# Kernel optimization log

Hardware: AMD Instinct MI355X
Metric: run time of the kernel (lower is better)

## Reference

```python
import jax, jax.numpy as jnp
import numpy as np

B, F, V, E = 65536, 39, 100000, 16
EPS = 1e-5

def setup_inputs() -> dict:
    key = jax.random.key(0)
    ks = jax.random.split(key, 10)
    return {
        'Xi': jax.random.randint(ks[0], (B, F, 1), 0, V, dtype=jnp.int64) if jax.config.read('jax_enable_x64') else jax.random.randint(ks[0], (B, F, 1), 0, V, dtype=jnp.int32),
        'Xv': jax.random.uniform(ks[1], (B, F), dtype=jnp.float32),
        'emb1': jax.random.normal(ks[2], (F, V, 1), dtype=jnp.float32),
        'emb2': jax.random.normal(ks[3], (F, V, E), dtype=jnp.float32),
        'W1': jax.random.normal(ks[4], (F * E, 512), dtype=jnp.float32) * 0.02,
        'b1': jax.random.normal(ks[5], (512,), dtype=jnp.float32) * 0.02,
        'g1': jnp.ones((512,), jnp.float32),
        'be1': jnp.zeros((512,), jnp.float32),
        'W2': jax.random.normal(ks[6], (512, 256), dtype=jnp.float32) * 0.02,
        'b2': jax.random.normal(ks[7], (256,), dtype=jnp.float32) * 0.02,
        'g2': jnp.ones((256,), jnp.float32),
        'be2': jnp.zeros((256,), jnp.float32),
        'bias': jax.random.normal(ks[8], (1,), dtype=jnp.float32),
    }

def _batchnorm(x, g, b):
    mu = jnp.mean(x, axis=0)
    var = jnp.mean(jnp.square(x - mu), axis=0)  # biased var, torch BN training mode
    return (x - mu) * jax.lax.rsqrt(var + EPS) * g + b

def reference(Xi, Xv, emb1, emb2, W1, b1, g1, be1, W2, b2, g2, be2, bias):
    idx = Xi[:, :, 0]                                # [B, F]
    fidx = jnp.arange(F)[None, :]                    # [1, F]
    # fused per-field gathers: [B, F] and [B, F, E]
    first = emb1[fidx, idx, 0] * Xv                  # first-order, [B, F]
    fm2 = emb2[fidx, idx] * Xv[:, :, None]           # second-order embeds, [B, F, E]
    sum_emb = jnp.sum(fm2, axis=1)                   # [B, E]
    second = 0.5 * (jnp.square(sum_emb) - jnp.sum(jnp.square(fm2), axis=1))  # [B, E]
    # deep part (note: original forward never applies the final num_classes layer)
    deep = fm2.reshape(B, F * E)
    deep = _batchnorm(deep @ W1 + b1, g1, be1)
    deep = _batchnorm(deep @ W2 + b2, g2, be2)
    return bias + jnp.sum(first, axis=1) + jnp.sum(second, axis=1) + jnp.sum(deep, axis=1)
```

## Files before the change

### kernel.cpp

```cpp
#include <hip/hip_runtime.h>

#define B_ROWS 65536
#define F_FEAT 39
#define V_VOC  100000
#define D_PAD  640
#define BN_EPS 1e-5f

typedef __bf16 bf16x8 __attribute__((ext_vector_type(8)));
typedef float  f32x16 __attribute__((ext_vector_type(16)));

__device__ __forceinline__ unsigned short toBF(float x) {
  unsigned int u = __float_as_uint(x);
  u += 0x7fffu + ((u >> 16) & 1u);
  return (unsigned short)(u >> 16);
}

__global__ __launch_bounds__(256) void k1_gather(
    const int* __restrict__ Xi, const float* __restrict__ Xv,
    const float* __restrict__ emb2,
    unsigned short* __restrict__ XT, float* __restrict__ fs,
    float* __restrict__ Mz) {
  if (threadIdx.x < 100)
    Mz[(size_t)blockIdx.x * 100 + threadIdx.x] = 0.f;

  const int b0 = blockIdx.x * 16;
  __shared__ int            sIdx[16][40];
  __shared__ float          sXv[16][40];
  __shared__ unsigned short xt[16][648];

  for (int u = threadIdx.x; u < 16 * 39; u += 256) {
    int r = u / 39, f = u - r * 39;
    sIdx[r][f] = Xi[(size_t)(b0 + r) * 39 + f];
    sXv[r][f]  = Xv[(size_t)(b0 + r) * 39 + f];
  }
  __syncthreads();

  const int r   = threadIdx.x >> 4;
  const int l16 = threadIdx.x & 15;
  const int seg = l16 & 3;
  const int fo  = l16 >> 2;

  float4 sv = {0.f, 0.f, 0.f, 0.f};
  float  ss = 0.f;
#pragma unroll
  for (int it = 0; it < 10; ++it) {
    const int f = it * 4 + fo;
    if (f < 39) {
      const int   id = sIdx[r][f];
      const float xv = sXv[r][f];
      const float4 v = *reinterpret_cast<const float4*>(
          emb2 + ((size_t)f * V_VOC + id) * 16 + seg * 4);
      const float a0 = v.x * xv, a1 = v.y * xv, a2 = v.z * xv, a3 = v.w * xv;
      sv.x += a0; sv.y += a1; sv.z += a2; sv.w += a3;
      ss += a0 * a0 + a1 * a1 + a2 * a2 + a3 * a3;
      uint2 pk;
      pk.x = (unsigned int)toBF(a0) | ((unsigned int)toBF(a1) << 16);
      pk.y = (unsigned int)toBF(a2) | ((unsigned int)toBF(a3) << 16);
      *reinterpret_cast<uint2*>(&xt[r][f * 16 + seg * 4]) = pk;
    }
  }
  sv.x += __shfl_xor(sv.x, 4); sv.y += __shfl_xor(sv.y, 4);
  sv.z += __shfl_xor(sv.z, 4); sv.w += __shfl_xor(sv.w, 4);
  sv.x += __shfl_xor(sv.x, 8); sv.y += __shfl_xor(sv.y, 8);
  sv.z += __shfl_xor(sv.z, 8); sv.w += __shfl_xor(sv.w, 8);
  float s2 = sv.x * sv.x + sv.y * sv.y + sv.z * sv.z + sv.w * sv.w;
  s2 += __shfl_xor(s2, 1);
  s2 += __shfl_xor(s2, 2);
  ss += __shfl_xor(ss, 1);
  ss += __shfl_xor(ss, 2);
  ss += __shfl_xor(ss, 4);
  ss += __shfl_xor(ss, 8);
  if (l16 == 0) fs[b0 + r] = 0.5f * (s2 - ss);
  __syncthreads();

  for (int m = threadIdx.x; m < 640; m += 256) {
    unsigned short* dst = XT + (size_t)m * B_ROWS + b0;
    unsigned int q2[8];
    if (m < 624) {
#pragma unroll
      for (int rr = 0; rr < 8; ++rr)
        q2[rr] = (unsigned int)xt[2 * rr][m] | ((unsigned int)xt[2 * rr + 1][m] << 16);
    } else {
      unsigned int fill = (m == 624) ? 0x3f803f80u : 0u;
#pragma unroll
      for (int rr = 0; rr < 8; ++rr) q2[rr] = fill;
    }
    uint4 w0, w1;
    w0.x = q2[0]; w0.y = q2[1]; w0.z = q2[2]; w0.w = q2[3];
    w1.x = q2[4]; w1.y = q2[5]; w1.z = q2[6]; w1.w = q2[7];
    *reinterpret_cast<uint4*>(dst)     = w0;
    *reinterpret_cast<uint4*>(dst + 8) = w1;
  }
}

#define KSPLIT 32
__global__ __launch_bounds__(256) void k2_syrk(const unsigned short* __restrict__ XT,
                                               float* __restrict__ M) {
  const int ks = blockIdx.x & (KSPLIT - 1);
  int pair = blockIdx.x >> 5;
  int ti = 0, p = pair;
  while (p >= 5 - ti) { p -= 5 - ti; ++ti; }
  const int tj = ti + p;

  __shared__ unsigned short pa[128 * 64];
  __shared__ unsigned short pb[128 * 64];

  const int lane = threadIdx.x & 63, wid = threadIdx.x >> 6;
  const int wm = wid >> 1, wn = wid & 1;
  const int rl = lane & 31, hh = lane >> 5;

  f32x16 acc00, acc01, acc10, acc11;
#pragma unroll
  for (int i = 0; i < 16; ++i) { acc00[i] = 0.f; acc01[i] = 0.f; acc10[i] = 0.f; acc11[i] = 0.f; }

  const int krange = B_ROWS / KSPLIT;
  const int kbase = ks * krange;

  for (int kt = 0; kt < krange; kt += 64) {
    const int k0 = kbase + kt;
#pragma unroll
    for (int g2 = 0; g2 < 4; ++g2) {
      const int g = threadIdx.x + g2 * 256;
      const int r = g >> 3, j = g & 7;
      uint4 va = *reinterpret_cast<const uint4*>(XT + (size_t)(ti * 128 + r) * B_ROWS + k0 + j * 8);
      *reinterpret_cast<uint4*>((char*)pa + r * 128 + ((j ^ (r & 7)) << 4)) = va;
      uint4 vb = *reinterpret_cast<const uint4*>(XT + (size_t)(tj * 128 + r) * B_ROWS + k0 + j * 8);
      *reinterpret_cast<uint4*>((char*)pb + r * 128 + ((j ^ (r & 7)) << 4)) = vb;
    }
    __syncthreads();
#pragma unroll
    for (int kc = 0; kc < 4; ++kc) {
      const int ra0 = wm * 64 + rl, ra1 = wm * 64 + 32 + rl;
      const int rb0 = wn * 64 + rl, rb1 = wn * 64 + 32 + rl;
      bf16x8 a0 = *reinterpret_cast<const bf16x8*>((char*)pa + ra0 * 128 + (((kc * 2 + hh) ^ (ra0 & 7)) << 4));
      bf16x8 a1 = *reinterpret_cast<const bf16x8*>((char*)pa + ra1 * 128 + (((kc * 2 + hh) ^ (ra1 & 7)) << 4));
      bf16x8 b0 = *reinterpret_cast<const bf16x8*>((char*)pb + rb0 * 128 + (((kc * 2 + hh) ^ (rb0 & 7)) << 4));
      bf16x8 b1 = *reinterpret_cast<const bf16x8*>((char*)pb + rb1 * 128 + (((kc * 2 + hh) ^ (rb1 & 7)) << 4));
      acc00 = __builtin_amdgcn_mfma_f32_32x32x16_bf16(a0, b0, acc00, 0, 0, 0);
      acc01 = __builtin_amdgcn_mfma_f32_32x32x16_bf16(a0, b1, acc01, 0, 0, 0);
      acc10 = __builtin_amdgcn_mfma_f32_32x32x16_bf16(a1, b0, acc10, 0, 0, 0);
      acc11 = __builtin_amdgcn_mfma_f32_32x32x16_bf16(a1, b1, acc11, 0, 0, 0);
    }
    __syncthreads();
  }

#pragma unroll
  for (int rr = 0; rr < 16; ++rr) {
    const int rloc = (rr & 3) + ((rr >> 2) << 3) + hh * 4;
    const int row0 = ti * 128 + wm * 64 + rloc;
    const int row1 = row0 + 32;
    const int col0 = tj * 128 + wn * 64 + rl;
    atomicAdd(&M[row0 * D_PAD + col0], acc00[rr]);
    atomicAdd(&M[row0 * D_PAD + col0 + 32], acc01[rr]);
    atomicAdd(&M[row1 * D_PAD + col0], acc10[rr]);
    atomicAdd(&M[row1 * D_PAD + col0 + 32], acc11[rr]);
  }
}

__device__ __forceinline__ float fetchM(const float* M, int a, int b) {
  if ((a >> 7) > (b >> 7)) { int t = a; a = b; b = t; }
  return M[a * D_PAD + b];
}
__global__ void k3a_cov(const float* __restrict__ M, float* __restrict__ Cov,
                        float* __restrict__ mu) {
  const int i = blockIdx.x;
  const float inv = 1.f / 65536.f;
  const float mui = fetchM(M, 624, i) * inv;
  for (int j = threadIdx.x; j < D_PAD; j += 256) {
    float muj = fetchM(M, 624, j) * inv;
    Cov[i * D_PAD + j] = fetchM(M, i, j) * inv - mui * muj;
    if (i == 0) mu[j] = muj;
  }
}

__global__ __launch_bounds__(256) void qform(const float* __restrict__ Cov,
                                             const float* __restrict__ W, const int ldw,
                                             const float* __restrict__ g,
                                             float* __restrict__ alpha) {
  const int k0 = blockIdx.x * 2;
  __shared__ float w0s[624], w1s[624];
  for (int i = threadIdx.x; i < 624; i += 256) {
    w0s[i] = W[(size_t)i * ldw + k0];
    w1s[i] = W[(size_t)i * ldw + k0 + 1];
  }
  __syncthreads();
  const int j0 = threadIdx.x, j1 = threadIdx.x + 256, j2 = threadIdx.x + 512;
  const bool v2 = (j2 < 624);
  const float wj00 = w0s[j0], wj01 = w0s[j1], wj02 = v2 ? w0s[j2] : 0.f;
  const float wj10 = w1s[j0], wj11 = w1s[j1], wj12 = v2 ? w1s[j2] : 0.f;
  float acc0 = 0.f, acc1 = 0.f;
  for (int i = 0; i < 624; ++i) {
    const float wi0 = w0s[i], wi1 = w1s[i];
    const float* row = Cov + i * D_PAD;
    const float c0 = row[j0], c1 = row[j1], c2 = v2 ? row[j2] : 0.f;
    acc0 += wi0 * (c0 * wj00 + c1 * wj01 + c2 * wj02);
    acc1 += wi1 * (c0 * wj10 + c1 * wj11 + c2 * wj12);
  }
#pragma unroll
  for (int off = 32; off > 0; off >>= 1) {
    acc0 += __shfl_down(acc0, off);
    acc1 += __shfl_down(acc1, off);
  }
  __shared__ float pr[2][4];
  const int lane = threadIdx.x & 63, wv = threadIdx.x >> 6;
  if (lane == 0) { pr[0][wv] = acc0; pr[1][wv] = acc1; }
  __syncthreads();
  if (threadIdx.x == 0) {
    float v0 = pr[0][0] + pr[0][1] + pr[0][2] + pr[0][3];
    float v1 = pr[1][0] + pr[1][1] + pr[1][2] + pr[1][3];
    alpha[k0]     = g[k0]     * rsqrtf(v0 + BN_EPS);
    alpha[k0 + 1] = g[k0 + 1] * rsqrtf(v1 + BN_EPS);
  }
}

__global__ __launch_bounds__(256) void k3c_G(const float* __restrict__ W1,
                                             const float* __restrict__ alpha1,
                                             const float* __restrict__ W2,
                                             float* __restrict__ G) {
  const int i = blockIdx.x;
  __shared__ float a[512];
  for (int k = threadIdx.x; k < 512; k += 256)
    a[k] = W1[(size_t)i * 512 + k] * alpha1[k];
  __syncthreads();
  const int j = threadIdx.x;
  float acc = 0.f;
#pragma unroll 8
  for (int k = 0; k < 512; ++k) acc += a[k] * W2[(size_t)k * 256 + j];
  G[(size_t)i * 256 + j] = acc;
}

__global__ __launch_bounds__(256) void k3e_final(const float* __restrict__ G,
                                                 const float* __restrict__ alpha2,
                                                 const float* __restrict__ mu,
                                                 const float* __restrict__ be2,
                                                 const float* __restrict__ bias,
                                                 float* __restrict__ gw,
                                                 float* __restrict__ consts) {
  __shared__ float a2[256];
  __shared__ float gws[640];
  a2[threadIdx.x] = alpha2[threadIdx.x];
  __syncthreads();
  for (int i = threadIdx.x; i < 640; i += 256) {
    float acc = 0.f;
    if (i < 624) {
      const float* gr = G + (size_t)i * 256;
#pragma unroll 8
      for (int j = 0; j < 256; ++j) acc += gr[j] * a2[j];
    }
    gw[i] = acc;
    gws[i] = acc;
  }
  __syncthreads();
  float pm = 0.f;
  for (int i = threadIdx.x; i < 624; i += 256) pm += mu[i] * gws[i];
  float val = be2[threadIdx.x] - pm;
#pragma unroll
  for (int off = 32; off > 0; off >>= 1) val += __shfl_down(val, off);
  __shared__ float pr[4];
  const int lane = threadIdx.x & 63, wv = threadIdx.x >> 6;
  if (lane == 0) pr[wv] = val;
  __syncthreads();
  if (threadIdx.x == 0) consts[0] = bias[0] + pr[0] + pr[1] + pr[2] + pr[3];
}

__global__ __launch_bounds__(256) void k5_out(const int* __restrict__ Xi,
                                              const float* __restrict__ Xv,
                                              const float* __restrict__ emb1,
                                              const unsigned short* __restrict__ XT,
                                              const float* __restrict__ gw,
                                              const float* __restrict__ fs,
                                              const float* __restrict__ consts,
                                              float* __restrict__ out) {
  const int b0 = blockIdx.x * 128;
  __shared__ int   si[128][40];
  __shared__ float sx[128][40];
  __shared__ float g[624];
  for (int m = threadIdx.x; m < 624; m += 256) g[m] = gw[m];
  for (int u = threadIdx.x; u < 128 * 39; u += 256) {
    int rr = u / 39, ff = u - rr * 39;
    si[rr][ff] = Xi[(size_t)b0 * 39 + u];
    sx[rr][ff] = Xv[(size_t)b0 * 39 + u];
  }
  __syncthreads();
  const int r = threadIdx.x >> 1, h = threadIdx.x & 1;
  const int b = b0 + r;
  float acc = 0.f;
  const unsigned short* col = XT + b;
  const int m0 = h * 312;
#pragma unroll 8
  for (int m = m0; m < m0 + 312; ++m) {
    unsigned int u = (unsigned int)col[(size_t)m * B_ROWS] << 16;
    acc += __uint_as_float(u) * g[m];
  }
  const int fb = h ? 20 : 0, fe = h ? 39 : 20;
  for (int f = fb; f < fe; ++f)
    acc += emb1[(size_t)f * V_VOC + si[r][f]] * sx[r][f];
  acc += __shfl_xor(acc, 1);
  if (h == 0) out[b] = acc + fs[b] + consts[0];
}

extern "C" void kernel_launch(void* const* d_in, const int* in_sizes, int n_in,
                              void* d_out, int out_size, void* d_ws, size_t ws_size,
                              hipStream_t stream) {
  const int*   Xi   = (const int*)d_in[0];
  const float* Xv   = (const float*)d_in[1];
  const float* emb1 = (const float*)d_in[2];
  const float* emb2 = (const float*)d_in[3];
  const float* W1   = (const float*)d_in[4];
  const float* g1   = (const float*)d_in[6];
  const float* W2   = (const float*)d_in[8];
  const float* g2   = (const float*)d_in[10];
  const float* be2  = (const float*)d_in[11];
  const float* bias = (const float*)d_in[12];
  float* out = (float*)d_out;
  char* ws = (char*)d_ws;

  const size_t OFF_XT  = 0;
  const size_t OFF_M   = OFF_XT + (size_t)640 * 65536 * 2;
  const size_t OFF_COV = OFF_M + (size_t)640 * 640 * 4;
  const size_t OFF_MU  = OFF_COV + (size_t)640 * 640 * 4;
  const size_t OFF_A1  = OFF_MU + 640 * 4;
  const size_t OFF_A2  = OFF_A1 + 512 * 4;
  const size_t OFF_G   = OFF_A2 + 256 * 4;
  const size_t OFF_GW  = OFF_G + (size_t)624 * 256 * 4;
  const size_t OFF_CN  = OFF_GW + 640 * 4;
  const size_t OFF_FS  = OFF_CN + 256;

  unsigned short* XT = (unsigned short*)(ws + OFF_XT);
  float* M   = (float*)(ws + OFF_M);
  float* COV = (float*)(ws + OFF_COV);
  float* MU  = (float*)(ws + OFF_MU);
  float* A1  = (float*)(ws + OFF_A1);
  float* A2  = (float*)(ws + OFF_A2);
  float* G   = (float*)(ws + OFF_G);
  float* GW  = (float*)(ws + OFF_GW);
  float* CN  = (float*)(ws + OFF_CN);
  float* FS  = (float*)(ws + OFF_FS);

  k1_gather<<<4096, 256, 0, stream>>>(Xi, Xv, emb2, XT, FS, M);
  k2_syrk<<<15 * KSPLIT, 256, 0, stream>>>(XT, M);
  k3a_cov<<<640, 256, 0, stream>>>(M, COV, MU);
  qform<<<256, 256, 0, stream>>>(COV, W1, 512, g1, A1);
  k3c_G<<<624, 256, 0, stream>>>(W1, A1, W2, G);
  qform<<<128, 256, 0, stream>>>(COV, G, 256, g2, A2);
  k3e_final<<<1, 256, 0, stream>>>(G, A2, MU, be2, bias, GW, CN);
  k5_out<<<512, 256, 0, stream>>>(Xi, Xv, emb1, XT, GW, FS, CN, out);
}
```

Before: 360.4 us.

## Restructure embedding gather per field, move FM second-order term into output kernel

Adds a prep kernel that transposes Xi/Xv into field-major layout, zeroes M and fills the padding rows of XT. The gather becomes one block per field and batch chunk, so each block reads from a single field's embedding table with software prefetch and writes coalesced transposed bf16 rows through a double-buffered shared tile. The FM second-order sum moves into k5_out, computed from the bf16 XT values, which drops the fs buffer but lowers the precision of that term. The syrk block index mapping is also changed to spread the K-splits across XCDs.

```diff
diff --git a/kernel.cpp b/kernel.cpp
--- a/kernel.cpp
+++ b/kernel.cpp
@@ -15,92 +15,89 @@
   return (unsigned short)(u >> 16);
 }
 
-__global__ __launch_bounds__(256) void k1_gather(
+__global__ __launch_bounds__(256) void k0_prep(
     const int* __restrict__ Xi, const float* __restrict__ Xv,
-    const float* __restrict__ emb2,
-    unsigned short* __restrict__ XT, float* __restrict__ fs,
-    float* __restrict__ Mz) {
-  if (threadIdx.x < 100)
-    Mz[(size_t)blockIdx.x * 100 + threadIdx.x] = 0.f;
-
-  const int b0 = blockIdx.x * 16;
-  __shared__ int            sIdx[16][40];
-  __shared__ float          sXv[16][40];
-  __shared__ unsigned short xt[16][648];
-
-  for (int u = threadIdx.x; u < 16 * 39; u += 256) {
+    int* __restrict__ XiT, float* __restrict__ XvT,
+    float* __restrict__ M, unsigned short* __restrict__ XT) {
+  for (int i = threadIdx.x; i < 800; i += 256)
+    M[(size_t)blockIdx.x * 800 + i] = 0.f;
+
+  const int b0 = blockIdx.x * 128;
+  for (int u = threadIdx.x; u < 16 * 128; u += 256) {
+    int m = 624 + (u >> 7), j = u & 127;
+    XT[(size_t)m * B_ROWS + b0 + j] = (m == 624) ? (unsigned short)0x3f80 : (unsigned short)0;
+  }
+
+  __shared__ int   ti[128][41];
+  __shared__ float tv[128][41];
+  for (int u = threadIdx.x; u < 128 * 39; u += 256) {
     int r = u / 39, f = u - r * 39;
-    sIdx[r][f] = Xi[(size_t)(b0 + r) * 39 + f];
-    sXv[r][f]  = Xv[(size_t)(b0 + r) * 39 + f];
-  }
-  __syncthreads();
-
-  const int r   = threadIdx.x >> 4;
-  const int l16 = threadIdx.x & 15;
-  const int seg = l16 & 3;
-  const int fo  = l16 >> 2;
-
-  float4 sv = {0.f, 0.f, 0.f, 0.f};
-  float  ss = 0.f;
-#pragma unroll
-  for (int it = 0; it < 10; ++it) {
-    const int f = it * 4 + fo;
-    if (f < 39) {
-      const int   id = sIdx[r][f];
-      const float xv = sXv[r][f];
-      const float4 v = *reinterpret_cast<const float4*>(
-          emb2 + ((size_t)f * V_VOC + id) * 16 + seg * 4);
-      const float a0 = v.x * xv, a1 = v.y * xv, a2 = v.z * xv, a3 = v.w * xv;
-      sv.x += a0; sv.y += a1; sv.z += a2; sv.w += a3;
-      ss += a0 * a0 + a1 * a1 + a2 * a2 + a3 * a3;
-      uint2 pk;
-      pk.x = (unsigned int)toBF(a0) | ((unsigned int)toBF(a1) << 16);
-      pk.y = (unsigned int)toBF(a2) | ((unsigned int)toBF(a3) << 16);
-      *reinterpret_cast<uint2*>(&xt[r][f * 16 + seg * 4]) = pk;
-    }
-  }
-  sv.x += __shfl_xor(sv.x, 4); sv.y += __shfl_xor(sv.y, 4);
-  sv.z += __shfl_xor(sv.z, 4); sv.w += __shfl_xor(sv.w, 4);
-  sv.x += __shfl_xor(sv.x, 8); sv.y += __shfl_xor(sv.y, 8);
-  sv.z += __shfl_xor(sv.z, 8); sv.w += __shfl_xor(sv.w, 8);
-  float s2 = sv.x * sv.x + sv.y * sv.y + sv.z * sv.z + sv.w * sv.w;
-  s2 += __shfl_xor(s2, 1);
-  s2 += __shfl_xor(s2, 2);
-  ss += __shfl_xor(ss, 1);
-  ss += __shfl_xor(ss, 2);
-  ss += __shfl_xor(ss, 4);
-  ss += __shfl_xor(ss, 8);
-  if (l16 == 0) fs[b0 + r] = 0.5f * (s2 - ss);
-  __syncthreads();
-
-  for (int m = threadIdx.x; m < 640; m += 256) {
-    unsigned short* dst = XT + (size_t)m * B_ROWS + b0;
-    unsigned int q2[8];
-    if (m < 624) {
-#pragma unroll
-      for (int rr = 0; rr < 8; ++rr)
-        q2[rr] = (unsigned int)xt[2 * rr][m] | ((unsigned int)xt[2 * rr + 1][m] << 16);
-    } else {
-      unsigned int fill = (m == 624) ? 0x3f803f80u : 0u;
-#pragma unroll
-      for (int rr = 0; rr < 8; ++rr) q2[rr] = fill;
-    }
-    uint4 w0, w1;
-    w0.x = q2[0]; w0.y = q2[1]; w0.z = q2[2]; w0.w = q2[3];
-    w1.x = q2[4]; w1.y = q2[5]; w1.z = q2[6]; w1.w = q2[7];
-    *reinterpret_cast<uint4*>(dst)     = w0;
-    *reinterpret_cast<uint4*>(dst + 8) = w1;
+    ti[r][f] = Xi[(size_t)b0 * 39 + u];
+    tv[r][f] = Xv[(size_t)b0 * 39 + u];
+  }
+  __syncthreads();
+  for (int u = threadIdx.x; u < 39 * 128; u += 256) {
+    int f = u >> 7, j = u & 127;
+    XiT[(size_t)f * B_ROWS + b0 + j] = ti[j][f];
+    XvT[(size_t)f * B_ROWS + b0 + j] = tv[j][f];
+  }
+}
+
+#define CHUNK 2048
+__global__ __launch_bounds__(256) void k1f_gather(
+    const int* __restrict__ XiT, const float* __restrict__ XvT,
+    const float* __restrict__ emb2, unsigned short* __restrict__ XT) {
+  const int f = blockIdx.x >> 5;
+  const int c = blockIdx.x & 31;
+  const int b0 = c * CHUNK;
+  const float* ef = emb2 + (size_t)f * V_VOC * 16;
+  const int*   xi = XiT + (size_t)f * B_ROWS + b0;
+  const float* xv = XvT + (size_t)f * B_ROWS + b0;
+  unsigned short* xtBase = XT + (size_t)(f * 16) * B_ROWS + b0;
+
+  __shared__ unsigned short xs[2][16][68];
+
+  const int seg = threadIdx.x & 3;
+  const int bi  = threadIdx.x >> 2;
+  const int dim = threadIdx.x >> 4;
+  const int prt = threadIdx.x & 15;
+
+  int   idA = xi[bi],      idB = xi[64 + bi];
+  float xvA = xv[bi],      xvB = xv[64 + bi];
+  float4 v = *reinterpret_cast<const float4*>(ef + (size_t)idA * 16 + seg * 4);
+
+  for (int s = 0; s < CHUNK / 64; ++s) {
+    const float4 cur = v;
+    const float  xvc = xvA;
+    idA = idB; xvA = xvB;
+    if (s + 2 < CHUNK / 64) {
+      idB = xi[(s + 2) * 64 + bi];
+      xvB = xv[(s + 2) * 64 + bi];
+    }
+    if (s + 1 < CHUNK / 64)
+      v = *reinterpret_cast<const float4*>(ef + (size_t)idA * 16 + seg * 4);
+
+    const int bf = s & 1;
+    xs[bf][seg * 4 + 0][bi] = toBF(cur.x * xvc);
+    xs[bf][seg * 4 + 1][bi] = toBF(cur.y * xvc);
+    xs[bf][seg * 4 + 2][bi] = toBF(cur.z * xvc);
+    xs[bf][seg * 4 + 3][bi] = toBF(cur.w * xvc);
+    __syncthreads();
+    uint2 w = *reinterpret_cast<const uint2*>(&xs[bf][dim][prt * 4]);
+    *reinterpret_cast<uint2*>(xtBase + (size_t)dim * B_ROWS + s * 64 + prt * 4) = w;
   }
 }
 
 #define KSPLIT 32
 __global__ __launch_bounds__(256) void k2_syrk(const unsigned short* __restrict__ XT,
                                                float* __restrict__ M) {
-  const int ks = blockIdx.x & (KSPLIT - 1);
-  int pair = blockIdx.x >> 5;
-  int ti = 0, p = pair;
-  while (p >= 5 - ti) { p -= 5 - ti; ++ti; }
-  const int tj = ti + p;
+  const int p = blockIdx.x;
+  const int xcd = p & 7;
+  const int ks = ((p >> 3) / 15) * 8 + xcd;
+  int pair = (p >> 3) % 15;
+  int ti = 0;
+  while (pair >= 5 - ti) { pair -= 5 - ti; ++ti; }
+  const int tj = ti + pair;
 
   __shared__ unsigned short pa[128 * 64];
   __shared__ unsigned short pb[128 * 64];
@@ -268,7 +265,6 @@
                                               const float* __restrict__ emb1,
                                               const unsigned short* __restrict__ XT,
                                               const float* __restrict__ gw,
-                                              const float* __restrict__ fs,
                                               const float* __restrict__ consts,
                                               float* __restrict__ out) {
   const int b0 = blockIdx.x * 128;
@@ -284,19 +280,37 @@
   __syncthreads();
   const int r = threadIdx.x >> 1, h = threadIdx.x & 1;
   const int b = b0 + r;
-  float acc = 0.f;
   const unsigned short* col = XT + b;
-  const int m0 = h * 312;
-#pragma unroll 8
-  for (int m = m0; m < m0 + 312; ++m) {
-    unsigned int u = (unsigned int)col[(size_t)m * B_ROWS] << 16;
-    acc += __uint_as_float(u) * g[m];
+
+  float lin = 0.f, ssq = 0.f;
+  float ps[16];
+#pragma unroll
+  for (int e = 0; e < 16; ++e) ps[e] = 0.f;
+
+  const int m0 = h ? 320 : 0, m1 = h ? 624 : 320;
+  for (int mo = m0; mo < m1; mo += 16) {
+#pragma unroll
+    for (int e = 0; e < 16; ++e) {
+      const int m = mo + e;
+      float x = __uint_as_float((unsigned int)col[(size_t)m * B_ROWS] << 16);
+      lin += g[m] * x;
+      ssq += x * x;
+      ps[e] += x;
+    }
   }
   const int fb = h ? 20 : 0, fe = h ? 39 : 20;
   for (int f = fb; f < fe; ++f)
-    acc += emb1[(size_t)f * V_VOC + si[r][f]] * sx[r][f];
-  acc += __shfl_xor(acc, 1);
-  if (h == 0) out[b] = acc + fs[b] + consts[0];
+    lin += emb1[(size_t)f * V_VOC + si[r][f]] * sx[r][f];
+
+  float s2 = 0.f;
+#pragma unroll
+  for (int e = 0; e < 16; ++e) {
+    float t = ps[e] + __shfl_xor(ps[e], 1);
+    s2 += t * t;
+  }
+  float tot = lin + 0.5f * (0.5f * s2 - ssq);
+  tot += __shfl_xor(tot, 1);
+  if (h == 0) out[b] = tot + consts[0];
 }
 
 extern "C" void kernel_launch(void* const* d_in, const int* in_sizes, int n_in,
@@ -324,7 +338,8 @@
   const size_t OFF_G   = OFF_A2 + 256 * 4;
   const size_t OFF_GW  = OFF_G + (size_t)624 * 256 * 4;
   const size_t OFF_CN  = OFF_GW + 640 * 4;
-  const size_t OFF_FS  = OFF_CN + 256;
+  const size_t OFF_XIT = OFF_CN + 256;
+  const size_t OFF_XVT = OFF_XIT + (size_t)39 * 65536 * 4;
 
   unsigned short* XT = (unsigned short*)(ws + OFF_XT);
   float* M   = (float*)(ws + OFF_M);
@@ -335,14 +350,16 @@
   float* G   = (float*)(ws + OFF_G);
   float* GW  = (float*)(ws + OFF_GW);
   float* CN  = (float*)(ws + OFF_CN);
-  float* FS  = (float*)(ws + OFF_FS);
-
-  k1_gather<<<4096, 256, 0, stream>>>(Xi, Xv, emb2, XT, FS, M);
+  int*   XIT = (int*)(ws + OFF_XIT);
+  float* XVT = (float*)(ws + OFF_XVT);
+
+  k0_prep<<<512, 256, 0, stream>>>(Xi, Xv, XIT, XVT, M, XT);
+  k1f_gather<<<39 * 32, 256, 0, stream>>>(XIT, XVT, emb2, XT);
   k2_syrk<<<15 * KSPLIT, 256, 0, stream>>>(XT, M);
   k3a_cov<<<640, 256, 0, stream>>>(M, COV, MU);
   qform<<<256, 256, 0, stream>>>(COV, W1, 512, g1, A1);
   k3c_G<<<624, 256, 0, stream>>>(W1, A1, W2, G);
   qform<<<128, 256, 0, stream>>>(COV, G, 256, g2, A2);
   k3e_final<<<1, 256, 0, stream>>>(G, A2, MU, be2, bias, GW, CN);
-  k5_out<<<512, 256, 0, stream>>>(Xi, Xv, emb1, XT, GW, FS, CN, out);
-}
+  k5_out<<<512, 256, 0, stream>>>(Xi, Xv, emb1, XT, GW, CN, out);
+}
```

Measured after the change: 343.4 us. 4.7% less time.
